# Kernel tuning notes

Measured on AMD Instinct MI355X. Metric: run time of the kernel, lower is better.

Reference implementation:

```python
import jax, jax.numpy as jnp
import numpy as np

EPS = 1e-5

def layernorm2d(x, w, b):
    # nn.LayerNorm([T, C]): normalize jointly over last two dims, affine shape [T, C]
    mu = jnp.mean(x, axis=(-2, -1), keepdims=True)
    var = jnp.mean(jnp.square(x - mu), axis=(-2, -1), keepdims=True)
    return (x - mu) * jax.lax.rsqrt(var + EPS) * w + b


def setup_inputs() -> dict:
    key = jax.random.key(0)
    ks = jax.random.split(key, 10)
    B, T, C = 64, 512, 512
    s = 0.02
    inputs = jax.random.normal(ks[0], (B, T, C), dtype=jnp.float32)
    ln1_w = jnp.ones((T, C), dtype=jnp.float32)
    ln1_b = jnp.zeros((T, C), dtype=jnp.float32)
    ln2_w = jnp.ones((T, C), dtype=jnp.float32)
    ln2_b = jnp.zeros((T, C), dtype=jnp.float32)
    # TriU: row i holds the Linear(i+1,1) weights for prefix 0..i -> lower-triangular [T,T]
    tri_M = jax.random.normal(ks[1], (T, T), dtype=jnp.float32) * s
    tri_b = jax.random.normal(ks[2], (T,), dtype=jnp.float32) * s
    d1_w = jax.random.normal(ks[3], (C, C), dtype=jnp.float32) * s  # dense_1: out = x @ d1_w.T + d1_b
    d1_b = jax.random.normal(ks[4], (C,), dtype=jnp.float32) * s
    d2_w = jax.random.normal(ks[5], (C, C), dtype=jnp.float32) * s
    d2_b = jax.random.normal(ks[6], (C,), dtype=jnp.float32) * s
    return {"inputs": inputs, "ln1_w": ln1_w, "ln1_b": ln1_b,
            "ln2_w": ln2_w, "ln2_b": ln2_b,
            "tri_M": tri_M, "tri_b": tri_b,
            "d1_w": d1_w, "d1_b": d1_b, "d2_w": d2_w, "d2_b": d2_b}


def reference(inputs, ln1_w, ln1_b, ln2_w, ln2_b, tri_M, tri_b, d1_w, d1_b, d2_w, d2_b):
    # x: [B, T, C]
    x = layernorm2d(inputs, ln1_w, ln1_b)
    # TriU time mixer: out[b,i,c] = sum_{j<=i} M[i,j] * x[b,j,c] + tri_b[i]
    M = jnp.tril(tri_M)
    x = jnp.einsum('it,btc->bic', M, x) + tri_b[None, :, None]
    x = layernorm2d(x + inputs, ln2_w, ln2_b)
    # channel mixer MLP (dropout = 0)
    h = jax.nn.gelu(jnp.einsum('btc,hc->bth', x, d1_w) + d1_b, approximate=False)
    y = jnp.einsum('bth,ch->btc', h, d2_w) + d2_b
    return x + y
```

## Files before the change

kernel.cpp:

```cpp
#include <hip/hip_runtime.h>
#include <hip/hip_bf16.h>
#include <math.h>


#define B_ 64
#define T_ 512
#define C_ 512
#define TC_ (T_ * C_)
static_assert(TC_ == 262144, "");

typedef __attribute__((ext_vector_type(8))) short bf16x8;
typedef __attribute__((ext_vector_type(4))) float f32x4;

__device__ __forceinline__ unsigned short f2bf(float f) {
  union { float f; unsigned u; } v; v.f = f;
  unsigned r = v.u + 0x7FFF + ((v.u >> 16) & 1);
  return (unsigned short)(r >> 16);
}
__device__ __forceinline__ float bf2f(unsigned short h) {
  union { unsigned u; float f; } v; v.u = ((unsigned)h) << 16; return v.f;
}

__device__ __forceinline__ void load16_lds(const void* gsrc, void* ldst) {
  __builtin_amdgcn_global_load_lds(
      (const __attribute__((address_space(1))) unsigned int*)gsrc,
      (__attribute__((address_space(3))) unsigned int*)ldst,
      16, 0, 0);
}

__global__ __launch_bounds__(256) void conv_weights(
    const float* __restrict__ triM, const float* __restrict__ d1w,
    const float* __restrict__ d2w, unsigned short* __restrict__ Mb,
    unsigned short* __restrict__ W1b, unsigned short* __restrict__ W2b) {
  const int idx = blockIdx.x * 256 + threadIdx.x;
  const int i = idx >> 9, j = idx & 511;
  Mb[idx]  = (j <= i) ? f2bf(triM[idx]) : (unsigned short)0;
  W1b[idx] = f2bf(d1w[idx]);
  W2b[idx] = f2bf(d2w[idx]);
}

__global__ __launch_bounds__(256) void ln_stats(const float* __restrict__ x,
                                                float* __restrict__ red) {
  const int b = blockIdx.x;
  const int s = blockIdx.y;
  const float4* p = (const float4*)(x + (size_t)b * TC_) + (size_t)s * 4096;
  float s1 = 0.f, s2 = 0.f;
  for (int i = threadIdx.x; i < 4096; i += 256) {
    float4 v = p[i];
    s1 += v.x + v.y + v.z + v.w;
    s2 += v.x * v.x + v.y * v.y + v.z * v.z + v.w * v.w;
  }
#pragma unroll
  for (int o = 32; o; o >>= 1) { s1 += __shfl_down(s1, o, 64); s2 += __shfl_down(s2, o, 64); }
  __shared__ float sm[8];
  const int w = threadIdx.x >> 6, lane = threadIdx.x & 63;
  if (lane == 0) { sm[w * 2] = s1; sm[w * 2 + 1] = s2; }
  __syncthreads();
  if (threadIdx.x == 0) {
    float a = 0.f, c = 0.f;
    for (int i = 0; i < 4; ++i) { a += sm[2 * i]; c += sm[2 * i + 1]; }
    atomicAdd(&red[b * 2], a);
    atomicAdd(&red[b * 2 + 1], c);
  }
}

__global__ __launch_bounds__(256) void ln1_norm_t(
    const float* __restrict__ x, const float* __restrict__ w,
    const float* __restrict__ bvec, const float* __restrict__ red1,
    unsigned short* __restrict__ XnT) {
  __shared__ unsigned short tile[64][65];
  const int b = blockIdx.z;
  const int t0 = blockIdx.y * 64;
  const int c0 = blockIdx.x * 64;
  const float mu = red1[b * 2] * (1.f / TC_);
  const float rstd = rsqrtf(red1[b * 2 + 1] * (1.f / TC_) - mu * mu + 1e-5f);
  const int tid = threadIdx.x;
  const int r = tid >> 4;
  const int cg = (tid & 15) * 4;
#pragma unroll
  for (int rr = 0; rr < 4; ++rr) {
    const int t = t0 + rr * 16 + r;
    const float4 xv = *(const float4*)&x[((size_t)b * T_ + t) * C_ + c0 + cg];
    const float4 wv = *(const float4*)&w[(size_t)t * C_ + c0 + cg];
    const float4 bv = *(const float4*)&bvec[(size_t)t * C_ + c0 + cg];
    tile[rr * 16 + r][cg + 0] = f2bf((xv.x - mu) * rstd * wv.x + bv.x);
    tile[rr * 16 + r][cg + 1] = f2bf((xv.y - mu) * rstd * wv.y + bv.y);
    tile[rr * 16 + r][cg + 2] = f2bf((xv.z - mu) * rstd * wv.z + bv.z);
    tile[rr * 16 + r][cg + 3] = f2bf((xv.w - mu) * rstd * wv.w + bv.w);
  }
  __syncthreads();
  const int cl = tid >> 2;
  const int tg = (tid & 3) * 16;
  alignas(16) unsigned short tmp[16];
#pragma unroll
  for (int j = 0; j < 16; ++j) tmp[j] = tile[tg + j][cl];
  unsigned short* o = &XnT[((size_t)b * C_ + c0 + cl) * T_ + t0 + tg];
  *(uint4*)&o[0] = *(const uint4*)&tmp[0];
  *(uint4*)&o[8] = *(const uint4*)&tmp[8];
}

__device__ __forceinline__ void gemm_mainloop(
    const unsigned short* __restrict__ Ag,
    const unsigned short* __restrict__ Bg,
    int lda, int ldb, int ktiles,
    unsigned short* Atile, unsigned short* Btile, f32x4 acc[4][4], int tid) {
  const int lane = tid & 63;
  const int w = tid >> 6;
  const int wr = (w >> 1) * 64;
  const int wc = (w & 1) * 64;
  const int m16 = lane & 15;
  const int quad = lane >> 4;
  for (int kt = 0; kt < ktiles; ++kt) {
    const int k0 = kt * 32;
#pragma unroll
    for (int i = 0; i < 2; ++i) {
      const int c = tid + 256 * i;
      const int row = c >> 2, ko = (c & 3) * 8;
      load16_lds(Ag + (size_t)row * lda + k0 + ko, Atile + c * 8);
      load16_lds(Bg + (size_t)row * ldb + k0 + ko, Btile + c * 8);
    }
    __syncthreads();
    bf16x8 af[4], bfr[4];
#pragma unroll
    for (int r = 0; r < 4; ++r)
      af[r] = *(const bf16x8*)&Atile[(wr + r * 16 + m16) * 32 + quad * 8];
#pragma unroll
    for (int c = 0; c < 4; ++c)
      bfr[c] = *(const bf16x8*)&Btile[(wc + c * 16 + m16) * 32 + quad * 8];
#pragma unroll
    for (int r = 0; r < 4; ++r)
#pragma unroll
      for (int c = 0; c < 4; ++c)
        acc[r][c] = __builtin_amdgcn_mfma_f32_16x16x32_bf16(af[r], bfr[c], acc[r][c], 0, 0, 0);
    __syncthreads();
  }
}

__global__ __launch_bounds__(256) void gemm_mixer(
    const unsigned short* __restrict__ Mb, const unsigned short* __restrict__ XnT,
    const float* __restrict__ trib, const float* __restrict__ inp,
    unsigned short* __restrict__ Z, float* __restrict__ red2) {
  __shared__ __align__(16) unsigned short Atile[4096], Btile[4096];
  const int b = blockIdx.z;
  const int i0 = blockIdx.y * 128;
  const int c0 = blockIdx.x * 128;
  f32x4 acc[4][4];
#pragma unroll
  for (int r = 0; r < 4; ++r)
#pragma unroll
    for (int c = 0; c < 4; ++c) acc[r][c] = (f32x4){0.f, 0.f, 0.f, 0.f};
  gemm_mainloop(Mb + (size_t)i0 * T_, XnT + (size_t)b * TC_ + (size_t)c0 * T_,
                T_, T_, (i0 >> 5) + 4, Atile, Btile, acc, threadIdx.x);
  const int tid = threadIdx.x, lane = tid & 63, w = tid >> 6;
  const int wr = (w >> 1) * 64, wc = (w & 1) * 64, m16 = lane & 15, quad = lane >> 4;
  float s1 = 0.f, s2 = 0.f;
#pragma unroll
  for (int r = 0; r < 4; ++r) {
#pragma unroll
    for (int g = 0; g < 4; ++g) {
      const int i = i0 + wr + r * 16 + quad * 4 + g;
      const float tb = trib[i];
      const float* inrow = &inp[((size_t)b * T_ + i) * C_];
      unsigned short* zrow = &Z[((size_t)b * T_ + i) * C_];
#pragma unroll
      for (int c = 0; c < 4; ++c) {
        const int ch = c0 + wc + c * 16 + m16;
        const float v = acc[r][c][g] + tb + inrow[ch];
        zrow[ch] = f2bf(v);
        s1 += v; s2 += v * v;
      }
    }
  }
#pragma unroll
  for (int o = 32; o; o >>= 1) { s1 += __shfl_down(s1, o, 64); s2 += __shfl_down(s2, o, 64); }
  __shared__ float sm[8];
  if (lane == 0) { sm[w * 2] = s1; sm[w * 2 + 1] = s2; }
  __syncthreads();
  if (tid == 0) {
    float a = 0.f, c2 = 0.f;
    for (int i = 0; i < 4; ++i) { a += sm[2 * i]; c2 += sm[2 * i + 1]; }
    atomicAdd(&red2[b * 2], a);
    atomicAdd(&red2[b * 2 + 1], c2);
  }
}

__global__ __launch_bounds__(256) void ln2_norm(
    const unsigned short* __restrict__ Z, const float* __restrict__ red2,
    const float* __restrict__ w, const float* __restrict__ bvec,
    unsigned short* __restrict__ X2) {
  const size_t e = ((size_t)blockIdx.x * 256 + threadIdx.x) * 8;
  const int b = (int)(e >> 18);
  const int tc = (int)(e & (TC_ - 1));
  const float mu = red2[b * 2] * (1.f / TC_);
  const float rstd = rsqrtf(red2[b * 2 + 1] * (1.f / TC_) - mu * mu + 1e-5f);
  uint4 zp = *(const uint4*)&Z[e];
  const unsigned short* zs = (const unsigned short*)&zp;
  alignas(16) float wv[8], bb[8];
  *(float4*)&wv[0] = *(const float4*)&w[tc];
  *(float4*)&wv[4] = *(const float4*)&w[tc + 4];
  *(float4*)&bb[0] = *(const float4*)&bvec[tc];
  *(float4*)&bb[4] = *(const float4*)&bvec[tc + 4];
  alignas(16) unsigned short o[8];
#pragma unroll
  for (int j = 0; j < 8; ++j)
    o[j] = f2bf((bf2f(zs[j]) - mu) * rstd * wv[j] + bb[j]);
  *(uint4*)&X2[e] = *(const uint4*)&o[0];
}

__global__ __launch_bounds__(256) void gemm_d1(
    const unsigned short* __restrict__ X2, const unsigned short* __restrict__ W1b,
    const float* __restrict__ d1b, unsigned short* __restrict__ H) {
  __shared__ __align__(16) unsigned short Atile[4096], Btile[4096];
  const int i0 = blockIdx.y * 128;
  const int n0 = blockIdx.x * 128;
  f32x4 acc[4][4];
#pragma unroll
  for (int r = 0; r < 4; ++r)
#pragma unroll
    for (int c = 0; c < 4; ++c) acc[r][c] = (f32x4){0.f, 0.f, 0.f, 0.f};
  gemm_mainloop(X2 + (size_t)i0 * C_, W1b + (size_t)n0 * C_, C_, C_, 16,
                Atile, Btile, acc, threadIdx.x);
  const int tid = threadIdx.x, lane = tid & 63, w = tid >> 6;
  const int wr = (w >> 1) * 64, wc = (w & 1) * 64, m16 = lane & 15, quad = lane >> 4;
#pragma unroll
  for (int r = 0; r < 4; ++r) {
#pragma unroll
    for (int g = 0; g < 4; ++g) {
      const int row = i0 + wr + r * 16 + quad * 4 + g;
#pragma unroll
      for (int c = 0; c < 4; ++c) {
        const int n = n0 + wc + c * 16 + m16;
        const float v = acc[r][c][g] + d1b[n];
        const float gl = 0.5f * v * (1.0f + erff(v * 0.70710678118654752f));
        H[(size_t)row * C_ + n] = f2bf(gl);
      }
    }
  }
}

__global__ __launch_bounds__(256) void gemm_d2(
    const unsigned short* __restrict__ H, const unsigned short* __restrict__ W2b,
    const float* __restrict__ d2b, const unsigned short* __restrict__ X2,
    float* __restrict__ out) {
  __shared__ __align__(16) unsigned short Atile[4096], Btile[4096];
  const int i0 = blockIdx.y * 128;
  const int n0 = blockIdx.x * 128;
  f32x4 acc[4][4];
#pragma unroll
  for (int r = 0; r < 4; ++r)
#pragma unroll
    for (int c = 0; c < 4; ++c) acc[r][c] = (f32x4){0.f, 0.f, 0.f, 0.f};
  gemm_mainloop(H + (size_t)i0 * C_, W2b + (size_t)n0 * C_, C_, C_, 16,
                Atile, Btile, acc, threadIdx.x);
  const int tid = threadIdx.x, lane = tid & 63, w = tid >> 6;
  const int wr = (w >> 1) * 64, wc = (w & 1) * 64, m16 = lane & 15, quad = lane >> 4;
#pragma unroll
  for (int r = 0; r < 4; ++r) {
#pragma unroll
    for (int g = 0; g < 4; ++g) {
      const int row = i0 + wr + r * 16 + quad * 4 + g;
#pragma unroll
      for (int c = 0; c < 4; ++c) {
        const int n = n0 + wc + c * 16 + m16;
        out[(size_t)row * C_ + n] = acc[r][c][g] + d2b[n] + bf2f(X2[(size_t)row * C_ + n]);
      }
    }
  }
}

extern "C" void kernel_launch(void* const* d_in, const int* in_sizes, int n_in,
                              void* d_out, int out_size, void* d_ws, size_t ws_size,
                              hipStream_t stream) {
  const float* inp  = (const float*)d_in[0];
  const float* ln1w = (const float*)d_in[1];
  const float* ln1b = (const float*)d_in[2];
  const float* ln2w = (const float*)d_in[3];
  const float* ln2b = (const float*)d_in[4];
  const float* triM = (const float*)d_in[5];
  const float* trib = (const float*)d_in[6];
  const float* d1w  = (const float*)d_in[7];
  const float* d1b  = (const float*)d_in[8];
  const float* d2w  = (const float*)d_in[9];
  const float* d2b  = (const float*)d_in[10];
  float* out = (float*)d_out;

  char* ws = (char*)d_ws;
  float* red1 = (float*)ws;
  float* red2 = (float*)(ws + 512);
  unsigned short* Mb  = (unsigned short*)(ws + 1024);
  unsigned short* W1b = Mb + TC_;
  unsigned short* W2b = W1b + TC_;
  unsigned short* XnT = W2b + TC_;
  unsigned short* Z   = XnT + (size_t)B_ * TC_;
  unsigned short* X2  = Z + (size_t)B_ * TC_;
  unsigned short* H   = X2 + (size_t)B_ * TC_;

  hipMemsetAsync(ws, 0, 1024, stream);
  conv_weights<<<1024, 256, 0, stream>>>(triM, d1w, d2w, Mb, W1b, W2b);
  ln_stats<<<dim3(B_, 16), 256, 0, stream>>>(inp, red1);
  ln1_norm_t<<<dim3(8, 8, B_), 256, 0, stream>>>(inp, ln1w, ln1b, red1, XnT);
  gemm_mixer<<<dim3(4, 4, B_), 256, 0, stream>>>(Mb, XnT, trib, inp, Z, red2);
  ln2_norm<<<8192, 256, 0, stream>>>(Z, red2, ln2w, ln2b, X2);
  gemm_d1<<<dim3(4, 256), 256, 0, stream>>>(X2, W1b, d1b, H);
  gemm_d2<<<dim3(4, 256), 256, 0, stream>>>(H, W2b, d2b, X2, out);
}
```

Before: 274.2 us.

## Load GEMM fragments directly from global memory with register double-buffering

Replaces the shared-memory staged GEMM main loop, which used global_load_lds with two barriers per k-tile, with a loop where each wave loads its MFMA operand fragments straight from global memory into registers. The next k-tile is prefetched into a second register set while the current one feeds the MFMAs. This removes LDS traffic and block-level synchronisation, but each of the two waves sharing a tile row or column now fetches the same data separately, which doubles global and L2 reads. It also raises register pressure.

```diff
diff --git a/kernel.cpp b/kernel.cpp
--- a/kernel.cpp
+++ b/kernel.cpp
@@ -19,13 +19,6 @@
 }
 __device__ __forceinline__ float bf2f(unsigned short h) {
   union { unsigned u; float f; } v; v.u = ((unsigned)h) << 16; return v.f;
-}
-
-__device__ __forceinline__ void load16_lds(const void* gsrc, void* ldst) {
-  __builtin_amdgcn_global_load_lds(
-      (const __attribute__((address_space(1))) unsigned int*)gsrc,
-      (__attribute__((address_space(3))) unsigned int*)ldst,
-      16, 0, 0);
 }
 
 __global__ __launch_bounds__(256) void conv_weights(
@@ -99,48 +92,56 @@
   *(uint4*)&o[8] = *(const uint4*)&tmp[8];
 }
 
-__device__ __forceinline__ void gemm_mainloop(
+__device__ __forceinline__ void gemm_direct(
     const unsigned short* __restrict__ Ag,
     const unsigned short* __restrict__ Bg,
-    int lda, int ldb, int ktiles,
-    unsigned short* Atile, unsigned short* Btile, f32x4 acc[4][4], int tid) {
+    int lda, int ldb, int ktiles, f32x4 acc[4][4], int tid) {
   const int lane = tid & 63;
   const int w = tid >> 6;
   const int wr = (w >> 1) * 64;
   const int wc = (w & 1) * 64;
   const int m16 = lane & 15;
   const int quad = lane >> 4;
-  for (int kt = 0; kt < ktiles; ++kt) {
-    const int k0 = kt * 32;
-#pragma unroll
-    for (int i = 0; i < 2; ++i) {
-      const int c = tid + 256 * i;
-      const int row = c >> 2, ko = (c & 3) * 8;
-      load16_lds(Ag + (size_t)row * lda + k0 + ko, Atile + c * 8);
-      load16_lds(Bg + (size_t)row * ldb + k0 + ko, Btile + c * 8);
-    }
-    __syncthreads();
-    bf16x8 af[4], bfr[4];
+  const unsigned short* ap[4];
+  const unsigned short* bp[4];
+#pragma unroll
+  for (int r = 0; r < 4; ++r)
+    ap[r] = Ag + (size_t)(wr + r * 16 + m16) * lda + quad * 8;
+#pragma unroll
+  for (int c = 0; c < 4; ++c)
+    bp[c] = Bg + (size_t)(wc + c * 16 + m16) * ldb + quad * 8;
+  bf16x8 a0[4], b0[4], a1[4], b1[4];
+#pragma unroll
+  for (int r = 0; r < 4; ++r) a0[r] = *(const bf16x8*)(ap[r]);
+#pragma unroll
+  for (int c = 0; c < 4; ++c) b0[c] = *(const bf16x8*)(bp[c]);
+  for (int kt = 0; kt < ktiles - 1; ++kt) {
+    const int ko = (kt + 1) * 32;
+#pragma unroll
+    for (int r = 0; r < 4; ++r) a1[r] = *(const bf16x8*)(ap[r] + ko);
+#pragma unroll
+    for (int c = 0; c < 4; ++c) b1[c] = *(const bf16x8*)(bp[c] + ko);
 #pragma unroll
     for (int r = 0; r < 4; ++r)
-      af[r] = *(const bf16x8*)&Atile[(wr + r * 16 + m16) * 32 + quad * 8];
+#pragma unroll
+      for (int c = 0; c < 4; ++c)
+        acc[r][c] = __builtin_amdgcn_mfma_f32_16x16x32_bf16(a0[r], b0[c], acc[r][c], 0, 0, 0);
+#pragma unroll
+    for (int r = 0; r < 4; ++r) a0[r] = a1[r];
+#pragma unroll
+    for (int c = 0; c < 4; ++c) b0[c] = b1[c];
+  }
+#pragma unroll
+  for (int r = 0; r < 4; ++r)
 #pragma unroll
     for (int c = 0; c < 4; ++c)
-      bfr[c] = *(const bf16x8*)&Btile[(wc + c * 16 + m16) * 32 + quad * 8];
-#pragma unroll
-    for (int r = 0; r < 4; ++r)
-#pragma unroll
-      for (int c = 0; c < 4; ++c)
-        acc[r][c] = __builtin_amdgcn_mfma_f32_16x16x32_bf16(af[r], bfr[c], acc[r][c], 0, 0, 0);
-    __syncthreads();
-  }
+      acc[r][c] = __builtin_amdgcn_mfma_f32_16x16x32_bf16(a0[r], b0[c], acc[r][c], 0, 0, 0);
 }
 
 __global__ __launch_bounds__(256) void gemm_mixer(
     const unsigned short* __restrict__ Mb, const unsigned short* __restrict__ XnT,
     const float* __restrict__ trib, const float* __restrict__ inp,
     unsigned short* __restrict__ Z, float* __restrict__ red2) {
-  __shared__ __align__(16) unsigned short Atile[4096], Btile[4096];
   const int b = blockIdx.z;
   const int i0 = blockIdx.y * 128;
   const int c0 = blockIdx.x * 128;
@@ -149,8 +150,8 @@
   for (int r = 0; r < 4; ++r)
 #pragma unroll
     for (int c = 0; c < 4; ++c) acc[r][c] = (f32x4){0.f, 0.f, 0.f, 0.f};
-  gemm_mainloop(Mb + (size_t)i0 * T_, XnT + (size_t)b * TC_ + (size_t)c0 * T_,
-                T_, T_, (i0 >> 5) + 4, Atile, Btile, acc, threadIdx.x);
+  gemm_direct(Mb + (size_t)i0 * T_, XnT + (size_t)b * TC_ + (size_t)c0 * T_,
+              T_, T_, (i0 >> 5) + 4, acc, threadIdx.x);
   const int tid = threadIdx.x, lane = tid & 63, w = tid >> 6;
   const int wr = (w >> 1) * 64, wc = (w & 1) * 64, m16 = lane & 15, quad = lane >> 4;
   float s1 = 0.f, s2 = 0.f;
@@ -210,7 +211,6 @@
 __global__ __launch_bounds__(256) void gemm_d1(
     const unsigned short* __restrict__ X2, const unsigned short* __restrict__ W1b,
     const float* __restrict__ d1b, unsigned short* __restrict__ H) {
-  __shared__ __align__(16) unsigned short Atile[4096], Btile[4096];
   const int i0 = blockIdx.y * 128;
   const int n0 = blockIdx.x * 128;
   f32x4 acc[4][4];
@@ -218,8 +218,8 @@
   for (int r = 0; r < 4; ++r)
 #pragma unroll
     for (int c = 0; c < 4; ++c) acc[r][c] = (f32x4){0.f, 0.f, 0.f, 0.f};
-  gemm_mainloop(X2 + (size_t)i0 * C_, W1b + (size_t)n0 * C_, C_, C_, 16,
-                Atile, Btile, acc, threadIdx.x);
+  gemm_direct(X2 + (size_t)i0 * C_, W1b + (size_t)n0 * C_, C_, C_, 16,
+              acc, threadIdx.x);
   const int tid = threadIdx.x, lane = tid & 63, w = tid >> 6;
   const int wr = (w >> 1) * 64, wc = (w & 1) * 64, m16 = lane & 15, quad = lane >> 4;
 #pragma unroll
@@ -242,7 +242,6 @@
     const unsigned short* __restrict__ H, const unsigned short* __restrict__ W2b,
     const float* __restrict__ d2b, const unsigned short* __restrict__ X2,
     float* __restrict__ out) {
-  __shared__ __align__(16) unsigned short Atile[4096], Btile[4096];
   const int i0 = blockIdx.y * 128;
   const int n0 = blockIdx.x * 128;
   f32x4 acc[4][4];
@@ -250,8 +249,8 @@
   for (int r = 0; r < 4; ++r)
 #pragma unroll
     for (int c = 0; c < 4; ++c) acc[r][c] = (f32x4){0.f, 0.f, 0.f, 0.f};
-  gemm_mainloop(H + (size_t)i0 * C_, W2b + (size_t)n0 * C_, C_, C_, 16,
-                Atile, Btile, acc, threadIdx.x);
+  gemm_direct(H + (size_t)i0 * C_, W2b + (size_t)n0 * C_, C_, C_, 16,
+              acc, threadIdx.x);
   const int tid = threadIdx.x, lane = tid & 63, w = tid >> 6;
   const int wr = (w >> 1) * 64, wc = (w & 1) * 64, m16 = lane & 15, quad = lane >> 4;
 #pragma unroll
```

New measurement: 368.0 us. 34.2% more time.
